# Kernel tuning notes

Measured on AMD Instinct MI355X. Metric: run time of the kernel, lower is better.

The kernel has to match this reference:

```python
import jax, jax.numpy as jnp
import numpy as np

NUM_LEVELS = 4
RADIUS = 4


def _avg_pool2(x):
    # x: [N, H, W] -> 2x2 avg pool, stride 2, VALID (matches F.avg_pool2d(corr, 2, 2))
    s = jax.lax.reduce_window(x, 0.0, jax.lax.add, (1, 2, 2), (1, 2, 2), 'VALID')
    return s * 0.25


def _bilinear_sampler(img, coords):
    # img: [N, H, W]; coords: [N, K, K, 2] with (x, y) in pixel units.
    # Matches grid_sample(align_corners=True, padding_mode='zeros').
    N, H, W = img.shape
    x, y = coords[..., 0], coords[..., 1]
    x0 = jnp.floor(x)
    y0 = jnp.floor(y)
    nidx = jnp.arange(N)[:, None, None]

    def corner(xi, yi, w):
        valid = (xi >= 0) & (xi <= W - 1) & (yi >= 0) & (yi <= H - 1)
        xc = jnp.clip(xi, 0, W - 1).astype(jnp.int32)
        yc = jnp.clip(yi, 0, H - 1).astype(jnp.int32)
        return jnp.where(valid, img[nidx, yc, xc], 0.0) * w

    wx1 = x - x0
    wx0 = 1.0 - wx1
    wy1 = y - y0
    wy0 = 1.0 - wy1
    return (corner(x0, y0, wx0 * wy0) + corner(x0 + 1.0, y0, wx1 * wy0)
            + corner(x0, y0 + 1.0, wx0 * wy1) + corner(x0 + 1.0, y0 + 1.0, wx1 * wy1))


def setup_inputs() -> dict:
    key = jax.random.key(0)
    ks = jax.random.split(key, 8)
    B, C, H, W, D = 2, 256, 46, 96, 256
    fmap1 = jax.random.normal(ks[0], (B, C, H, W), jnp.float32)
    fmap2 = jax.random.normal(ks[1], (B, C, H, W), jnp.float32)
    ys, xs = jnp.meshgrid(jnp.arange(H, dtype=jnp.float32),
                          jnp.arange(W, dtype=jnp.float32), indexing='ij')
    base = jnp.broadcast_to(jnp.stack([xs, ys], 0), (B, 2, H, W))  # channels = (x, y)
    coords1 = base
    coords_lookup = base + 2.0 * jax.random.normal(ks[2], (B, 2, H, W), jnp.float32)
    Wf = jax.random.normal(ks[3], (C, D), jnp.float32) / np.sqrt(C).astype(np.float32)
    bf = jnp.zeros((D,), jnp.float32)
    Wpos = jax.random.normal(ks[4], (2, D), jnp.float32) * 0.003
    Wq = jax.random.normal(ks[5], (D, D), jnp.float32) / np.sqrt(D).astype(np.float32)
    Wk = jax.random.normal(ks[6], (D, D), jnp.float32) / np.sqrt(D).astype(np.float32)
    return {"fmap1": fmap1, "fmap2": fmap2, "coords1": coords1,
            "coords_lookup": coords_lookup, "Wf": Wf, "bf": bf,
            "Wpos": Wpos, "Wq": Wq, "Wk": Wk}


def reference(fmap1, fmap2, coords1, coords_lookup, Wf, bf, Wpos, Wq, Wk):
    B, C, H, W = fmap1.shape
    HW = H * W
    D = Wf.shape[1]
    dt = fmap1.dtype
    # --- update(): SETrans cross-attention correlation volume ---
    # coords2 = gen_all_indices -> full (y, x) grid
    ys, xs = jnp.meshgrid(jnp.arange(H, dtype=dt), jnp.arange(W, dtype=dt), indexing='ij')
    coords2_yx = jnp.broadcast_to(jnp.stack([ys, xs], -1), (B, H, W, 2)).reshape(B, HW, 2)
    # coords1 stored as (x, y) channels; permute(0,2,3,1).flip(-1) -> (y, x)
    coords1_yx = jnp.transpose(coords1, (0, 2, 3, 1))[..., ::-1].reshape(B, HW, 2)
    f1 = jnp.transpose(fmap1.reshape(B, C, HW), (0, 2, 1))  # [B, HW, C]
    f2 = jnp.transpose(fmap2.reshape(B, C, HW), (0, 2, 1))
    pos1 = coords1_yx @ Wpos                                  # [B, HW, D]
    pos2 = coords2_yx @ Wpos
    vispos1 = f1 @ Wf + bf + pos1
    vispos2 = f2 @ Wf + bf + pos2
    scale = jnp.sqrt(jnp.asarray(D, dt))
    pos_biases = jnp.einsum('bid,bjd->bij', pos1, pos2) / scale  # injected positional biases
    q = vispos1 @ Wq
    k = vispos2 @ Wk
    scores = jnp.einsum('bid,bjd->bij', q, k) / scale + pos_biases
    corr = jax.nn.softmax(scores, axis=-1)                    # [B, HW1, HW2] attn-prob correlation
    corr = corr.reshape(B * HW, H, W)
    pyramid = [corr]
    for _ in range(NUM_LEVELS - 1):
        corr = _avg_pool2(corr)
        pyramid.append(corr)
    # --- __call__(coords): multiscale bilinear lookup ---
    r = RADIUS
    d = jnp.linspace(-r, r, 2 * r + 1, dtype=dt)
    dyy, dxx = jnp.meshgrid(d, d, indexing='ij')              # matches torch.meshgrid(dy, dx)
    delta = jnp.stack([dyy, dxx], -1)[None]                   # [1, K, K, 2]
    cl = jnp.transpose(coords_lookup, (0, 2, 3, 1)).reshape(B * HW, 1, 1, 2)
    outs = []
    for i, lvl in enumerate(pyramid):
        coords_lvl = cl / (2.0 ** i) + delta                  # [B*HW, K, K, 2]
        samp = _bilinear_sampler(lvl, coords_lvl)             # [B*HW, K, K]
        outs.append(samp.reshape(B, H, W, -1))
    out = jnp.concatenate(outs, axis=-1)                      # [B, H, W, L*K*K]
    return jnp.transpose(out, (0, 3, 1, 2)).astype(jnp.float32)
```

## Files before the change

kernel.cpp:

```cpp
#include <hip/hip_runtime.h>
#include <cstdint>

typedef _Float16 f16;
typedef __attribute__((ext_vector_type(2))) _Float16 f16x2;
typedef __attribute__((ext_vector_type(4))) _Float16 f16x4;
typedef __attribute__((ext_vector_type(8))) _Float16 f16x8;
typedef __attribute__((ext_vector_type(4))) float f32x4;

#define NB 2
#define NH 46
#define NW 96
#define NHW 4416
#define ND 256
#define NTILES 276
#define SSTR 4424
#define L2E 1.44269504f

#define OFF_WFQ 0
#define OFF_WFK 131072
#define OFF_PQ  262144
#define OFF_PK  264192
#define OFF_BQ  266240
#define OFF_BK  267264
#define OFF_GS  268288
#define OFF_Q   268544
#define OFF_K   4790528
#define OFF_RM  9312512
#define OFF_S   9453824
#define SCOL    4432
#define WS_NEED 87740672UL

__global__ __launch_bounds__(256) void prep_kernel(
    const float* __restrict__ Wf, const float* __restrict__ bf,
    const float* __restrict__ Wpos, const float* __restrict__ Wq,
    const float* __restrict__ Wk, char* __restrict__ ws) {
  f16* WFQ = (f16*)(ws + OFF_WFQ);
  f16* WFK = (f16*)(ws + OFF_WFK);
  float* PQ = (float*)(ws + OFF_PQ);
  float* PK = (float*)(ws + OFF_PK);
  float* BQ = (float*)(ws + OFF_BQ);
  float* BK = (float*)(ws + OFF_BK);
  float* GS = (float*)(ws + OFF_GS);
  int bid = blockIdx.x, d = threadIdx.x;
  if (bid < 256) {
    int c = bid;
    float aq = 0.f, ak = 0.f;
    for (int t = 0; t < 256; ++t) {
      float wf = Wf[c * 256 + t];
      aq += wf * Wq[t * 256 + d];
      ak += wf * Wk[t * 256 + d];
    }
    WFQ[c * 256 + d] = (f16)(aq * 0.0625f);
    WFK[c * 256 + d] = (f16)ak;
  } else if (bid == 256) {
    float pq0 = 0, pq1 = 0, pk0 = 0, pk1 = 0, bq = 0, bk = 0;
    for (int c = 0; c < 256; ++c) {
      float wq = Wq[c * 256 + d], wk = Wk[c * 256 + d];
      pq0 += Wpos[c] * wq;       pq1 += Wpos[256 + c] * wq;
      pk0 += Wpos[c] * wk;       pk1 += Wpos[256 + c] * wk;
      bq  += bf[c] * wq;         bk  += bf[c] * wk;
    }
    PQ[d] = pq0 * 0.0625f; PQ[256 + d] = pq1 * 0.0625f;
    PK[d] = pk0;           PK[256 + d] = pk1;
    BQ[d] = bq * 0.0625f;  BK[d] = bk;
  } else if (d < 4) {
    int a = d >> 1, b2 = d & 1;
    float g = 0;
    for (int t = 0; t < 256; ++t) g += Wpos[a * 256 + t] * Wpos[b2 * 256 + t];
    GS[d] = g * 0.0625f;
  }
}

__global__ __launch_bounds__(256) void qk_gemm(
    const float* __restrict__ fmap1, const float* __restrict__ fmap2,
    const float* __restrict__ coords1, char* __restrict__ ws) {
  __shared__ f16 As[64 * 40];
  __shared__ f16 Bs[128 * 40];
  __shared__ float py[64], px[64];
  const int z = blockIdx.z;
  const float* fmap = z ? fmap2 : fmap1;
  const f16* Wt = (const f16*)(ws + (z ? OFF_WFK : OFF_WFQ));
  const float* P = (const float*)(ws + (z ? OFF_PK : OFF_PQ));
  const float* bias = (const float*)(ws + (z ? OFF_BK : OFF_BQ));
  f16* outb = (f16*)(ws + (z ? OFF_K : OFF_Q));
  const int t = threadIdx.x;
  const int g0 = blockIdx.x * 64;
  const int b = g0 / NHW;
  const int hwb = g0 - b * NHW;
  const int d0 = blockIdx.y * 128;
  if (t < 64) {
    int hw = hwb + t;
    if (z == 0) {
      py[t] = coords1[(b * 2 + 1) * NHW + hw];
      px[t] = coords1[(b * 2 + 0) * NHW + hw];
    } else {
      int y = hw / NW;
      py[t] = (float)y;
      px[t] = (float)(hw - y * NW);
    }
  }
  const int lane = t & 63, wave = t >> 6;
  const int wr = (wave >> 1) * 32, wc0 = (wave & 1) * 64;
  const int hwl = t & 63, cl0 = t >> 6;
  const int dd = t & 127, ch = t >> 7;
  f32x4 acc[2][4] = {};
  for (int kt = 0; kt < 8; ++kt) {
    int kk = kt * 32;
    __syncthreads();
#pragma unroll
    for (int i = 0; i < 8; ++i) {
      int c = cl0 + i * 4;
      As[hwl * 40 + c] = (f16)fmap[(size_t)(b * ND + kk + c) * NHW + hwb + hwl];
    }
#pragma unroll
    for (int i = 0; i < 16; ++i) {
      int c = ch * 16 + i;
      Bs[dd * 40 + c] = Wt[(kk + c) * ND + d0 + dd];
    }
    __syncthreads();
    int row = lane & 15, kq = (lane >> 4) * 8;
    f16x8 a0 = *(const f16x8*)&As[(wr + row) * 40 + kq];
    f16x8 a1 = *(const f16x8*)&As[(wr + 16 + row) * 40 + kq];
#pragma unroll
    for (int s = 0; s < 4; ++s) {
      f16x8 bs = *(const f16x8*)&Bs[(wc0 + 16 * s + row) * 40 + kq];
      acc[0][s] = __builtin_amdgcn_mfma_f32_16x16x32_f16(a0, bs, acc[0][s], 0, 0, 0);
      acc[1][s] = __builtin_amdgcn_mfma_f32_16x16x32_f16(a1, bs, acc[1][s], 0, 0, 0);
    }
  }
#pragma unroll
  for (int fi = 0; fi < 2; ++fi)
#pragma unroll
    for (int s = 0; s < 4; ++s)
#pragma unroll
      for (int r = 0; r < 4; ++r) {
        int rowl = wr + fi * 16 + (lane >> 4) * 4 + r;
        int d = d0 + wc0 + s * 16 + (lane & 15);
        float v = acc[fi][s][r] + bias[d] + py[rowl] * P[d] + px[rowl] * P[ND + d];
        outb[(size_t)(g0 + rowl) * ND + d] = (f16)v;
      }
}

__global__ __launch_bounds__(384, 2) void score_gemm(
    const float* __restrict__ coords1, char* __restrict__ ws) {
  __shared__ f16 kls[2][32][264];
  __shared__ f16 stw[6][16][36];
  __shared__ float u0s[96], u1s[96];
  const int tid = threadIdx.x;
  const int blk = blockIdx.x;
  const int xcd = blk & 7;
  const int b = xcd >> 2, nq = xcd & 3;
  const int hw0 = (blk >> 3) * 96;
  const int j00 = nq * 1104;
  const float* GS = (const float*)(ws + OFF_GS);
  if (tid < 96) {
    int hw = hw0 + tid;
    float cy = coords1[(b * 2 + 1) * NHW + hw];
    float cx = coords1[(b * 2 + 0) * NHW + hw];
    u0s[tid] = cy * GS[0] + cx * GS[2];
    u1s[tid] = cy * GS[1] + cx * GS[3];
  }
  const f16* __restrict__ qb = (const f16*)(ws + OFF_Q);
  const f16* __restrict__ kb = (const f16*)(ws + OFF_K);
  f16* __restrict__ gSb = (f16*)(ws + OFF_S) + ((size_t)b * NHW + hw0) * SCOL;
  float* __restrict__ rmG = (float*)(ws + OFF_RM);
  const int lane = tid & 63, wave = tid >> 6;
  const int q = lane & 15, h = lane >> 4;
  f16x8 qfrag[8];
#pragma unroll
  for (int ks = 0; ks < 8; ++ks)
    qfrag[ks] = *(const f16x8*)&qb[(size_t)(b * NHW + hw0 + wave * 16 + q) * ND + ks * 32 + h * 8];
  for (int c = tid; c < 32 * 32; c += 384) {
    int r = c >> 5, cc = c & 31;
    *(f16x8*)&kls[0][r][cc * 8] =
        *(const f16x8*)&kb[(size_t)(b * NHW + j00 + r) * ND + cc * 8];
  }
  __syncthreads();
  const float u0m = u0s[wave * 16 + q], u1m = u1s[wave * 16 + q];
  float pmax = -3e38f;
  const int srow = lane >> 2, scg = lane & 3;

  for (int it = 0; it <= 34; ++it) {
    const int buf = it & 1;
    const int jp = j00 + it * 32;
    const bool full = (it < 34);
    if (it < 34) {
      const int nW = (it < 33) ? 32 : 16;
      const int jn = j00 + (it + 1) * 32;
      for (int c = tid; c < nW * 32; c += 384) {
        int r = c >> 5, cc = c & 31;
        *(f16x8*)&kls[buf ^ 1][r][cc * 8] =
            *(const f16x8*)&kb[(size_t)(b * NHW + jn + r) * ND + cc * 8];
      }
    }
    f32x4 acc0 = {}, acc1 = {};
#pragma unroll
    for (int ks = 0; ks < 8; ++ks) {
      f16x8 kf = *(const f16x8*)&kls[buf][q][ks * 32 + h * 8];
      acc0 = __builtin_amdgcn_mfma_f32_16x16x32_f16(kf, qfrag[ks], acc0, 0, 0, 0);
    }
    if (full) {
#pragma unroll
      for (int ks = 0; ks < 8; ++ks) {
        f16x8 kf = *(const f16x8*)&kls[buf][16 + q][ks * 32 + h * 8];
        acc1 = __builtin_amdgcn_mfma_f32_16x16x32_f16(kf, qfrag[ks], acc1, 0, 0, 0);
      }
    }
    {
      f16x4 v0, v1;
#pragma unroll
      for (int r = 0; r < 4; ++r) {
        int j = jp + h * 4 + r;
        int yj = j / NW;
        float s = acc0[r] + u0m * (float)yj + u1m * (float)(j - yj * NW);
        pmax = fmaxf(pmax, s);
        v0[r] = (f16)s;
      }
      *(f16x4*)&stw[wave][q][h * 4] = v0;
      if (full) {
#pragma unroll
        for (int r = 0; r < 4; ++r) {
          int j = jp + 16 + h * 4 + r;
          int yj = j / NW;
          float s = acc1[r] + u0m * (float)yj + u1m * (float)(j - yj * NW);
          pmax = fmaxf(pmax, s);
          v1[r] = (f16)s;
        }
        *(f16x4*)&stw[wave][q][16 + h * 4] = v1;
      }
    }
    if (full) {
      f16x8 row8 = *(const f16x8*)&stw[wave][srow][scg * 8];
      *(f16x8*)&gSb[(size_t)(wave * 16 + srow) * SCOL + jp + scg * 8] = row8;
    } else {
      f16x4 row4 = *(const f16x4*)&stw[wave][srow][scg * 4];
      *(f16x4*)&gSb[(size_t)(wave * 16 + srow) * SCOL + jp + scg * 4] = row4;
    }
    __syncthreads();
  }
  pmax = fmaxf(pmax, __shfl_xor(pmax, 16));
  pmax = fmaxf(pmax, __shfl_xor(pmax, 32));
  if (lane < 16)
    rmG[((size_t)b * 4 + nq) * NHW + hw0 + wave * 16 + q] = pmax;
}

__global__ __launch_bounds__(512) void lookup_kernel(
    const float* __restrict__ clup, const char* __restrict__ ws,
    float* __restrict__ out) {
  __shared__ f16 lv1[4][1104];
  __shared__ f16 lv2[4][264];
  __shared__ f16 lv3[4][60];
  __shared__ float wpart[8];
  __shared__ float clxs[16], clys[16], rinv[16], rm[16];
  const int tid = threadIdx.x;
  const int blk0 = blockIdx.x;
  const int xcd = blk0 & 7;
  const int b = xcd >> 2;
  const int hw0 = ((blk0 >> 3) * 4 + (xcd & 3)) * 16;
  const f16* gS = (const f16*)(ws + OFF_S);
  const float* rmG = (const float*)(ws + OFF_RM);
  if (tid < 16) {
    int hw = hw0 + tid;
    clxs[tid] = clup[(b * 2 + 0) * NHW + hw];
    clys[tid] = clup[(b * 2 + 1) * NHW + hw];
    const float* rp = rmG + (size_t)b * 4 * NHW + hw;
    rm[tid] = fmaxf(fmaxf(rp[0], rp[NHW]), fmaxf(rp[2 * NHW], rp[3 * NHW]));
  }
  __syncthreads();
  const int lane = tid & 63, wave = tid >> 6;
  const int rgrp = tid >> 7, ts = tid & 127;
  for (int p = 0; p < 4; ++p) {
    const int r = p * 4 + rgrp;
    const f16* sp = gS + (size_t)(b * NHW + hw0 + r) * SCOL;
    const float m = rm[r];
    float psum = 0.f;
    for (int cp = ts; cp < 552; cp += 128) {
      int c = cp * 2;
      int yy = c / 48, xx = c - yy * 48;
      f16x4 a = *(const f16x4*)&sp[(2 * yy) * NW + 2 * xx];
      f16x4 bb = *(const f16x4*)&sp[(2 * yy + 1) * NW + 2 * xx];
      float e0 = __builtin_amdgcn_exp2f(((float)a[0] - m) * L2E);
      float e1 = __builtin_amdgcn_exp2f(((float)a[1] - m) * L2E);
      float e2 = __builtin_amdgcn_exp2f(((float)bb[0] - m) * L2E);
      float e3 = __builtin_amdgcn_exp2f(((float)bb[1] - m) * L2E);
      float e4 = __builtin_amdgcn_exp2f(((float)a[2] - m) * L2E);
      float e5 = __builtin_amdgcn_exp2f(((float)a[3] - m) * L2E);
      float e6 = __builtin_amdgcn_exp2f(((float)bb[2] - m) * L2E);
      float e7 = __builtin_amdgcn_exp2f(((float)bb[3] - m) * L2E);
      float sA = (e0 + e1) + (e2 + e3);
      float sB = (e4 + e5) + (e6 + e7);
      f16x2 w2; w2[0] = (f16)sA; w2[1] = (f16)sB;
      *(f16x2*)&lv1[rgrp][c] = w2;
      psum += sA + sB;
    }
#pragma unroll
    for (int off = 1; off < 64; off <<= 1) psum += __shfl_xor(psum, off);
    if (lane == 0) wpart[wave] = psum;
    __syncthreads();
    if (tid < 4)
      rinv[p * 4 + tid] = 1.f / (wpart[2 * tid] + wpart[2 * tid + 1]);
    for (int c2 = ts; c2 < 264; c2 += 128) {
      int yy = c2 / 24, xx = c2 - yy * 24;
      f16x2 a = *(const f16x2*)&lv1[rgrp][(2 * yy) * 48 + 2 * xx];
      f16x2 bb = *(const f16x2*)&lv1[rgrp][(2 * yy + 1) * 48 + 2 * xx];
      lv2[rgrp][c2] = (f16)(((float)a[0] + (float)a[1]) + ((float)bb[0] + (float)bb[1]));
    }
    __syncthreads();
    if (ts < 60) {
      int yy = ts / 12, xx = ts - yy * 12;
      f16x2 a = *(const f16x2*)&lv2[rgrp][(2 * yy) * 24 + 2 * xx];
      f16x2 bb = *(const f16x2*)&lv2[rgrp][(2 * yy + 1) * 24 + 2 * xx];
      lv3[rgrp][ts] = (f16)(((float)a[0] + (float)a[1]) + ((float)bb[0] + (float)bb[1]));
    }
    __syncthreads();
    for (int idx = tid; idx < 1296; idx += 512) {
      int rl = idx / 324, c = idx - rl * 324;
      int rr = p * 4 + rl;
      int lvl = c / 81, rem = c - lvl * 81;
      int k0 = rem / 9, k1 = rem - k0 * 9;
      const float wdiv[4] = {1.f, 0.25f, 0.0625f, 0.015625f};
      const int Wi[4] = {96, 48, 24, 12}, Hi[4] = {46, 23, 11, 5};
      float m2 = rm[rr];
      const f16* spq = gS + (size_t)(b * NHW + hw0 + rr) * SCOL;
      float xq = clxs[rr] / (float)(1 << lvl) + (float)(k0 - 4);
      float yq = clys[rr] / (float)(1 << lvl) + (float)(k1 - 4);
      float x0f = floorf(xq), y0f = floorf(yq);
      int x0 = (int)x0f, y0 = (int)y0f;
      float wx1 = xq - x0f, wx0 = 1.f - wx1;
      float wy1 = yq - y0f, wy0 = 1.f - wy1;
      int Wl = Wi[lvl], Hl = Hi[lvl];
      float v = 0.f;
#pragma unroll
      for (int dy = 0; dy < 2; ++dy)
#pragma unroll
        for (int dx = 0; dx < 2; ++dx) {
          int xi = x0 + dx, yi = y0 + dy;
          if (xi >= 0 && xi < Wl && yi >= 0 && yi < Hl) {
            float pv;
            if (lvl == 0)
              pv = __builtin_amdgcn_exp2f(((float)spq[yi * NW + xi] - m2) * L2E);
            else if (lvl == 1) pv = (float)lv1[rl][yi * 48 + xi];
            else if (lvl == 2) pv = (float)lv2[rl][yi * 24 + xi];
            else               pv = (float)lv3[rl][yi * 12 + xi];
            v += pv * (dx ? wx1 : wx0) * (dy ? wy1 : wy0);
          }
        }
      int hw = hw0 + rr;
      int h = hw / NW, w = hw - h * NW;
      int chn = lvl * 81 + k0 * 9 + k1;
      out[((size_t)(b * 324 + chn) * NH + h) * NW + w] = v * wdiv[lvl] * rinv[rr];
    }
    __syncthreads();
  }
}

__global__ __launch_bounds__(1024) void attn_lookup(
    const float* __restrict__ coords1, const float* __restrict__ clup,
    const char* __restrict__ ws, float* __restrict__ out) {
  __shared__ f16 S[16 * SSTR];
  __shared__ f16 lv1[4][1104];
  __shared__ f16 lv2[4][264];
  __shared__ f16 lv3[4][60];
  __shared__ float wmax[16][16];
  __shared__ float wpart[16];
  __shared__ float u0s[16], u1s[16], clxs[16], clys[16], rinv[16], rowmaxS[16];
  const int tid = threadIdx.x;
  const int blk0 = blockIdx.x;
  const int xcd = blk0 & 7;
  const int b = xcd >> 2;
  const int hw0 = ((blk0 >> 3) * 4 + (xcd & 3)) * 16;
  const float* GS = (const float*)(ws + OFF_GS);
  if (tid < 16) {
    int hw = hw0 + tid;
    float cy = coords1[(b * 2 + 1) * NHW + hw];
    float cx = coords1[(b * 2 + 0) * NHW + hw];
    u0s[tid] = cy * GS[0] + cx * GS[2];
    u1s[tid] = cy * GS[1] + cx * GS[3];
    clxs[tid] = clup[(b * 2 + 0) * NHW + hw];
    clys[tid] = clup[(b * 2 + 1) * NHW + hw];
  }
  const f16* qb = (const f16*)(ws + OFF_Q);
  const f16* kb = (const f16*)(ws + OFF_K);
  const int lane = tid & 63;
  const int arow = lane & 15, akq = (lane >> 4) * 8;
  const int i0 = (lane >> 4) * 4;
  f16x8 afrag[8];
#pragma unroll
  for (int ks = 0; ks < 8; ++ks)
    afrag[ks] = *(const f16x8*)&qb[(size_t)(b * NHW + hw0 + arow) * ND + ks * 32 + akq];
  __syncthreads();
  float u0r[4], u1r[4];
#pragma unroll
  for (int r = 0; r < 4; ++r) { u0r[r] = u0s[i0 + r]; u1r[r] = u1s[i0 + r]; }
  const int wave = tid >> 6;
  float pmax[4] = {-3e38f, -3e38f, -3e38f, -3e38f};
  {
    const int cnt = (NTILES - wave + 15) / 16;
    const f16* kp = &kb[(size_t)(b * NHW + wave * 16 + arow) * ND + akq];
    const size_t tstep = (size_t)256 * ND;
    int nt = wave;
    f16x8 h0[4], h1[4];
#pragma unroll
    for (int s = 0; s < 4; ++s) h0[s] = *(const f16x8*)&kp[s * 32];
    for (int i = 0; i < cnt; ++i) {
      f32x4 acc0 = {}, acc1 = {};
// ... 87 lines not shown
      const float wdiv[4] = {1.f, 0.25f, 0.0625f, 0.015625f};
      const int Wi[4] = {96, 48, 24, 12}, Hi[4] = {46, 23, 11, 5};
      float m2 = rowmaxS[rr];
      float xq = clxs[rr] / (float)(1 << lvl) + (float)(k0 - 4);
      float yq = clys[rr] / (float)(1 << lvl) + (float)(k1 - 4);
      float x0f = floorf(xq), y0f = floorf(yq);
      int x0 = (int)x0f, y0 = (int)y0f;
      float wx1 = xq - x0f, wx0 = 1.f - wx1;
      float wy1 = yq - y0f, wy0 = 1.f - wy1;
      int Wl = Wi[lvl], Hl = Hi[lvl];
      float v = 0.f;
#pragma unroll
      for (int dy = 0; dy < 2; ++dy)
#pragma unroll
        for (int dx = 0; dx < 2; ++dx) {
          int xi = x0 + dx, yi = y0 + dy;
          if (xi >= 0 && xi < Wl && yi >= 0 && yi < Hl) {
            float pv;
            if (lvl == 0)
              pv = __builtin_amdgcn_exp2f(((float)S[rr * SSTR + yi * NW + xi] - m2) * L2E);
            else if (lvl == 1) pv = (float)lv1[rl][yi * 48 + xi];
            else if (lvl == 2) pv = (float)lv2[rl][yi * 24 + xi];
            else               pv = (float)lv3[rl][yi * 12 + xi];
            v += pv * (dx ? wx1 : wx0) * (dy ? wy1 : wy0);
          }
        }
      int hw = hw0 + rr;
      int h = hw / NW, w = hw - h * NW;
      int chn = lvl * 81 + k0 * 9 + k1;
      out[((size_t)(b * 324 + chn) * NH + h) * NW + w] = v * wdiv[lvl] * rinv[rr];
    }
    __syncthreads();
  }
}

extern "C" void kernel_launch(void* const* d_in, const int* in_sizes, int n_in,
                              void* d_out, int out_size, void* d_ws, size_t ws_size,
                              hipStream_t stream) {
  const float* fmap1 = (const float*)d_in[0];
  const float* fmap2 = (const float*)d_in[1];
  const float* coords1 = (const float*)d_in[2];
  const float* clup = (const float*)d_in[3];
  const float* Wf = (const float*)d_in[4];
  const float* bf = (const float*)d_in[5];
  const float* Wpos = (const float*)d_in[6];
  const float* Wq = (const float*)d_in[7];
  const float* Wk = (const float*)d_in[8];
  char* ws = (char*)d_ws;
  float* out = (float*)d_out;

  prep_kernel<<<dim3(258), dim3(256), 0, stream>>>(Wf, bf, Wpos, Wq, Wk, ws);
  qk_gemm<<<dim3(138, 2, 2), dim3(256), 0, stream>>>(fmap1, fmap2, coords1, ws);
  if (ws_size >= (size_t)WS_NEED) {
    score_gemm<<<dim3(46 * 8), dim3(384), 0, stream>>>(coords1, ws);
    lookup_kernel<<<dim3(NB * NTILES), dim3(512), 0, stream>>>(clup, ws, out);
  } else {
    attn_lookup<<<dim3(NB * NTILES), dim3(1024), 0, stream>>>(coords1, clup, ws, out);
  }
}
```

Before: 153.3 us.

## Give each score_gemm wave two query tiles and store K in fragment-native LDS layout

score_gemm now runs 3 waves instead of 6, and each wave owns 32 query rows, so every K fragment loaded from LDS feeds two MFMAs. K is staged in a pre-swizzled fragment-order layout, which lets each lane read one contiguous f16x8 without padded row indexing. The score tile writeback and row-max reduction are widened to match. Separately, the prep_kernel loops get unroll pragmas. Halving the threads per block lowers latency hiding and raises register pressure from the doubled q fragments and accumulators.

Result: slower. 188.0 us (+22.6%).

```diff
diff --git a/kernel.cpp b/kernel.cpp
--- a/kernel.cpp
+++ b/kernel.cpp
@@ -45,6 +45,7 @@
   if (bid < 256) {
     int c = bid;
     float aq = 0.f, ak = 0.f;
+#pragma unroll 8
     for (int t = 0; t < 256; ++t) {
       float wf = Wf[c * 256 + t];
       aq += wf * Wq[t * 256 + d];
@@ -54,6 +55,7 @@
     WFK[c * 256 + d] = (f16)ak;
   } else if (bid == 256) {
     float pq0 = 0, pq1 = 0, pk0 = 0, pk1 = 0, bq = 0, bk = 0;
+#pragma unroll 4
     for (int c = 0; c < 256; ++c) {
       float wq = Wq[c * 256 + d], wk = Wk[c * 256 + d];
       pq0 += Wpos[c] * wq;       pq1 += Wpos[256 + c] * wq;
@@ -141,10 +143,10 @@
       }
 }
 
-__global__ __launch_bounds__(384, 2) void score_gemm(
+__global__ __launch_bounds__(192, 2) void score_gemm(
     const float* __restrict__ coords1, char* __restrict__ ws) {
-  __shared__ f16 kls[2][32][264];
-  __shared__ f16 stw[6][16][36];
+  __shared__ f16x8 klsF[2][1024];
+  __shared__ f16 stw[3][32][40];
   __shared__ float u0s[96], u1s[96];
   const int tid = threadIdx.x;
   const int blk = blockIdx.x;
@@ -165,83 +167,94 @@
   f16* __restrict__ gSb = (f16*)(ws + OFF_S) + ((size_t)b * NHW + hw0) * SCOL;
   float* __restrict__ rmG = (float*)(ws + OFF_RM);
   const int lane = tid & 63, wave = tid >> 6;
-  const int q = lane & 15, h = lane >> 4;
-  f16x8 qfrag[8];
-#pragma unroll
-  for (int ks = 0; ks < 8; ++ks)
-    qfrag[ks] = *(const f16x8*)&qb[(size_t)(b * NHW + hw0 + wave * 16 + q) * ND + ks * 32 + h * 8];
-  for (int c = tid; c < 32 * 32; c += 384) {
-    int r = c >> 5, cc = c & 31;
-    *(f16x8*)&kls[0][r][cc * 8] =
-        *(const f16x8*)&kb[(size_t)(b * NHW + j00 + r) * ND + cc * 8];
+  const int lq = lane & 15, h = lane >> 4;
+  const int wq0 = wave * 32;
+  f16x8 qfrag[2][8];
+#pragma unroll
+  for (int s = 0; s < 2; ++s)
+#pragma unroll
+    for (int ks = 0; ks < 8; ++ks)
+      qfrag[s][ks] = *(const f16x8*)&qb[(size_t)(b * NHW + hw0 + wq0 + s * 16 + lq) * ND + ks * 32 + h * 8];
+  for (int c = tid; c < 1024; c += 192) {
+    int half = c >> 9, u = c & 511, ks = u >> 6, l = u & 63;
+    int r = half * 16 + (l & 15), col = ks * 32 + (l >> 4) * 8;
+    klsF[0][c] = *(const f16x8*)&kb[(size_t)(b * NHW + j00 + r) * ND + col];
   }
   __syncthreads();
-  const float u0m = u0s[wave * 16 + q], u1m = u1s[wave * 16 + q];
-  float pmax = -3e38f;
-  const int srow = lane >> 2, scg = lane & 3;
+  const float u0a = u0s[wq0 + lq], u1a = u1s[wq0 + lq];
+  const float u0b = u0s[wq0 + 16 + lq], u1b = u1s[wq0 + 16 + lq];
+  float pmax0 = -3e38f, pmax1 = -3e38f;
+  const int srow = lane >> 1, scg = lane & 1;
 
   for (int it = 0; it <= 34; ++it) {
     const int buf = it & 1;
     const int jp = j00 + it * 32;
     const bool full = (it < 34);
     if (it < 34) {
-      const int nW = (it < 33) ? 32 : 16;
+      const int nC = (it < 33) ? 1024 : 512;
       const int jn = j00 + (it + 1) * 32;
-      for (int c = tid; c < nW * 32; c += 384) {
-        int r = c >> 5, cc = c & 31;
-        *(f16x8*)&kls[buf ^ 1][r][cc * 8] =
-            *(const f16x8*)&kb[(size_t)(b * NHW + jn + r) * ND + cc * 8];
-      }
-    }
-    f32x4 acc0 = {}, acc1 = {};
+      for (int c = tid; c < nC; c += 192) {
+        int half = c >> 9, u = c & 511, ks = u >> 6, l = u & 63;
+        int r = half * 16 + (l & 15), col = ks * 32 + (l >> 4) * 8;
+        klsF[buf ^ 1][c] = *(const f16x8*)&kb[(size_t)(b * NHW + jn + r) * ND + col];
+      }
+    }
+    f32x4 acc[2][2] = {};
 #pragma unroll
     for (int ks = 0; ks < 8; ++ks) {
-      f16x8 kf = *(const f16x8*)&kls[buf][q][ks * 32 + h * 8];
-      acc0 = __builtin_amdgcn_mfma_f32_16x16x32_f16(kf, qfrag[ks], acc0, 0, 0, 0);
+      f16x8 k0 = klsF[buf][ks * 64 + lane];
+      acc[0][0] = __builtin_amdgcn_mfma_f32_16x16x32_f16(k0, qfrag[0][ks], acc[0][0], 0, 0, 0);
+      acc[0][1] = __builtin_amdgcn_mfma_f32_16x16x32_f16(k0, qfrag[1][ks], acc[0][1], 0, 0, 0);
     }
     if (full) {
 #pragma unroll
       for (int ks = 0; ks < 8; ++ks) {
-        f16x8 kf = *(const f16x8*)&kls[buf][16 + q][ks * 32 + h * 8];
-        acc1 = __builtin_amdgcn_mfma_f32_16x16x32_f16(kf, qfrag[ks], acc1, 0, 0, 0);
-      }
-    }
-    {
+        f16x8 k1 = klsF[buf][512 + ks * 64 + lane];
+        acc[1][0] = __builtin_amdgcn_mfma_f32_16x16x32_f16(k1, qfrag[0][ks], acc[1][0], 0, 0, 0);
+        acc[1][1] = __builtin_amdgcn_mfma_f32_16x16x32_f16(k1, qfrag[1][ks], acc[1][1], 0, 0, 0);
+      }
+    }
+    const int na = full ? 2 : 1;
+    for (int a = 0; a < na; ++a) {
+      float yf[4], xf[4];
+#pragma unroll
+      for (int r = 0; r < 4; ++r) {
+        int j = jp + a * 16 + h * 4 + r;
+        int yj = j / NW;
+        yf[r] = (float)yj; xf[r] = (float)(j - yj * NW);
+      }
       f16x4 v0, v1;
 #pragma unroll
       for (int r = 0; r < 4; ++r) {
-        int j = jp + h * 4 + r;
-        int yj = j / NW;
-        float s = acc0[r] + u0m * (float)yj + u1m * (float)(j - yj * NW);
-        pmax = fmaxf(pmax, s);
-        v0[r] = (f16)s;
-      }
-      *(f16x4*)&stw[wave][q][h * 4] = v0;
-      if (full) {
-#pragma unroll
-        for (int r = 0; r < 4; ++r) {
-          int j = jp + 16 + h * 4 + r;
-          int yj = j / NW;
-          float s = acc1[r] + u0m * (float)yj + u1m * (float)(j - yj * NW);
-          pmax = fmaxf(pmax, s);
-          v1[r] = (f16)s;
-        }
-        *(f16x4*)&stw[wave][q][16 + h * 4] = v1;
-      }
+        float s0 = acc[a][0][r] + u0a * yf[r] + u1a * xf[r];
+        float s1 = acc[a][1][r] + u0b * yf[r] + u1b * xf[r];
+        pmax0 = fmaxf(pmax0, s0);
+        pmax1 = fmaxf(pmax1, s1);
+        v0[r] = (f16)s0; v1[r] = (f16)s1;
+      }
+      *(f16x4*)&stw[wave][lq][a * 16 + h * 4] = v0;
+      *(f16x4*)&stw[wave][16 + lq][a * 16 + h * 4] = v1;
     }
     if (full) {
+#pragma unroll
+      for (int g = 0; g < 2; ++g) {
+        f16x8 row8 = *(const f16x8*)&stw[wave][srow][(scg * 2 + g) * 8];
+        *(f16x8*)&gSb[(size_t)(wq0 + srow) * SCOL + jp + (scg * 2 + g) * 8] = row8;
+      }
+    } else {
       f16x8 row8 = *(const f16x8*)&stw[wave][srow][scg * 8];
-      *(f16x8*)&gSb[(size_t)(wave * 16 + srow) * SCOL + jp + scg * 8] = row8;
-    } else {
-      f16x4 row4 = *(const f16x4*)&stw[wave][srow][scg * 4];
-      *(f16x4*)&gSb[(size_t)(wave * 16 + srow) * SCOL + jp + scg * 4] = row4;
-    }
-    __syncthreads();
-  }
-  pmax = fmaxf(pmax, __shfl_xor(pmax, 16));
-  pmax = fmaxf(pmax, __shfl_xor(pmax, 32));
-  if (lane < 16)
-    rmG[((size_t)b * 4 + nq) * NHW + hw0 + wave * 16 + q] = pmax;
+      *(f16x8*)&gSb[(size_t)(wq0 + srow) * SCOL + jp + scg * 8] = row8;
+    }
+    __syncthreads();
+  }
+  pmax0 = fmaxf(pmax0, __shfl_xor(pmax0, 16));
+  pmax0 = fmaxf(pmax0, __shfl_xor(pmax0, 32));
+  pmax1 = fmaxf(pmax1, __shfl_xor(pmax1, 16));
+  pmax1 = fmaxf(pmax1, __shfl_xor(pmax1, 32));
+  if (lane < 16) {
+    rmG[((size_t)b * 4 + nq) * NHW + hw0 + wq0 + lq] = pmax0;
+    rmG[((size_t)b * 4 + nq) * NHW + hw0 + wq0 + 16 + lq] = pmax1;
+  }
 }
 
 __global__ __launch_bounds__(512) void lookup_kernel(
@@ -544,7 +557,7 @@
   prep_kernel<<<dim3(258), dim3(256), 0, stream>>>(Wf, bf, Wpos, Wq, Wk, ws);
   qk_gemm<<<dim3(138, 2, 2), dim3(256), 0, stream>>>(fmap1, fmap2, coords1, ws);
   if (ws_size >= (size_t)WS_NEED) {
-    score_gemm<<<dim3(46 * 8), dim3(384), 0, stream>>>(coords1, ws);
+    score_gemm<<<dim3(46 * 8), dim3(192), 0, stream>>>(coords1, ws);
     lookup_kernel<<<dim3(NB * NTILES), dim3(512), 0, stream>>>(clup, ws, out);
   } else {
     attn_lookup<<<dim3(NB * NTILES), dim3(1024), 0, stream>>>(coords1, clup, ws, out);
```

## Fuse level-1 pooling and lookup window extraction into score GEMM epilogue

Applied to the files above, without the earlier changes.

The score GEMM no longer writes the full fp16 score matrix to global memory. It processes two image rows at a time, computes per-row-pair maxima, writes exp-pooled level-1 values, and copies a 16x16 window of raw scores around each lookup point. The lookup kernel then rescales level 1 with the per-pair maxima and samples level 0 from that window, which removes a large global write and read in exchange for more epilogue work and extra synchronisation in the GEMM. The prep loops also get unroll pragmas.

Result: slower. 203.2 us (+32.5%).

```diff
diff --git a/kernel.cpp b/kernel.cpp
--- a/kernel.cpp
+++ b/kernel.cpp
@@ -25,10 +25,10 @@
 #define OFF_GS  268288
 #define OFF_Q   268544
 #define OFF_K   4790528
-#define OFF_RM  9312512
-#define OFF_S   9453824
-#define SCOL    4432
-#define WS_NEED 87740672UL
+#define OFF_MP  9312512
+#define OFF_WIN 10160384
+#define OFF_L1  14682368
+#define WS_NEED 35031296UL
 
 __global__ __launch_bounds__(256) void prep_kernel(
     const float* __restrict__ Wf, const float* __restrict__ bf,
@@ -45,6 +45,7 @@
   if (bid < 256) {
     int c = bid;
     float aq = 0.f, ak = 0.f;
+#pragma unroll 8
     for (int t = 0; t < 256; ++t) {
       float wf = Wf[c * 256 + t];
       aq += wf * Wq[t * 256 + d];
@@ -54,6 +55,7 @@
     WFK[c * 256 + d] = (f16)ak;
   } else if (bid == 256) {
     float pq0 = 0, pq1 = 0, pk0 = 0, pk1 = 0, bq = 0, bk = 0;
+#pragma unroll 4
     for (int c = 0; c < 256; ++c) {
       float wq = Wq[c * 256 + d], wk = Wk[c * 256 + d];
       pq0 += Wpos[c] * wq;       pq1 += Wpos[256 + c] * wq;
@@ -142,16 +144,22 @@
 }
 
 __global__ __launch_bounds__(384, 2) void score_gemm(
-    const float* __restrict__ coords1, char* __restrict__ ws) {
+    const float* __restrict__ coords1, const float* __restrict__ clup,
+    char* __restrict__ ws) {
   __shared__ f16 kls[2][32][264];
-  __shared__ f16 stw[6][16][36];
+  __shared__ f16 Sbuf[96][200];
   __shared__ float u0s[96], u1s[96];
+  __shared__ float mrowL[96];
+  __shared__ float clwx[96], clwy[96];
   const int tid = threadIdx.x;
   const int blk = blockIdx.x;
   const int xcd = blk & 7;
   const int b = xcd >> 2, nq = xcd & 3;
   const int hw0 = (blk >> 3) * 96;
-  const int j00 = nq * 1104;
+  const int y0q = nq * 12;
+  const int j00 = y0q * NW;
+  const int npairs = (nq == 3) ? 5 : 6;
+  const int G = npairs * 6;
   const float* GS = (const float*)(ws + OFF_GS);
   if (tid < 96) {
     int hw = hw0 + tid;
@@ -159,35 +167,36 @@
     float cx = coords1[(b * 2 + 0) * NHW + hw];
     u0s[tid] = cy * GS[0] + cx * GS[2];
     u1s[tid] = cy * GS[1] + cx * GS[3];
+    clwx[tid] = clup[(b * 2 + 0) * NHW + hw];
+    clwy[tid] = clup[(b * 2 + 1) * NHW + hw];
   }
   const f16* __restrict__ qb = (const f16*)(ws + OFF_Q);
   const f16* __restrict__ kb = (const f16*)(ws + OFF_K);
-  f16* __restrict__ gSb = (f16*)(ws + OFF_S) + ((size_t)b * NHW + hw0) * SCOL;
-  float* __restrict__ rmG = (float*)(ws + OFF_RM);
+  float* __restrict__ mpG = (float*)(ws + OFF_MP);
+  f16* __restrict__ winG = (f16*)(ws + OFF_WIN);
+  f16* __restrict__ l1G = (f16*)(ws + OFF_L1);
   const int lane = tid & 63, wave = tid >> 6;
-  const int q = lane & 15, h = lane >> 4;
+  const int lq = lane & 15, h = lane >> 4;
+  const int wq0 = wave * 16;
   f16x8 qfrag[8];
 #pragma unroll
   for (int ks = 0; ks < 8; ++ks)
-    qfrag[ks] = *(const f16x8*)&qb[(size_t)(b * NHW + hw0 + wave * 16 + q) * ND + ks * 32 + h * 8];
-  for (int c = tid; c < 32 * 32; c += 384) {
+    qfrag[ks] = *(const f16x8*)&qb[(size_t)(b * NHW + hw0 + wq0 + lq) * ND + ks * 32 + h * 8];
+  for (int c = tid; c < 1024; c += 384) {
     int r = c >> 5, cc = c & 31;
     *(f16x8*)&kls[0][r][cc * 8] =
         *(const f16x8*)&kb[(size_t)(b * NHW + j00 + r) * ND + cc * 8];
   }
   __syncthreads();
-  const float u0m = u0s[wave * 16 + q], u1m = u1s[wave * 16 + q];
+  const float u0m = u0s[wq0 + lq], u1m = u1s[wq0 + lq];
   float pmax = -3e38f;
-  const int srow = lane >> 2, scg = lane & 3;
-
-  for (int it = 0; it <= 34; ++it) {
-    const int buf = it & 1;
-    const int jp = j00 + it * 32;
-    const bool full = (it < 34);
-    if (it < 34) {
-      const int nW = (it < 33) ? 32 : 16;
-      const int jn = j00 + (it + 1) * 32;
-      for (int c = tid; c < nW * 32; c += 384) {
+
+  for (int g = 0; g < G; ++g) {
+    const int buf = g & 1;
+    const int jp = j00 + g * 32;
+    if (g + 1 < G) {
+      const int jn = j00 + (g + 1) * 32;
+      for (int c = tid; c < 1024; c += 384) {
         int r = c >> 5, cc = c & 31;
         *(f16x8*)&kls[buf ^ 1][r][cc * 8] =
             *(const f16x8*)&kb[(size_t)(b * NHW + jn + r) * ND + cc * 8];
@@ -196,52 +205,75 @@
     f32x4 acc0 = {}, acc1 = {};
 #pragma unroll
     for (int ks = 0; ks < 8; ++ks) {
-      f16x8 kf = *(const f16x8*)&kls[buf][q][ks * 32 + h * 8];
-      acc0 = __builtin_amdgcn_mfma_f32_16x16x32_f16(kf, qfrag[ks], acc0, 0, 0, 0);
-    }
-    if (full) {
-#pragma unroll
-      for (int ks = 0; ks < 8; ++ks) {
-        f16x8 kf = *(const f16x8*)&kls[buf][16 + q][ks * 32 + h * 8];
-        acc1 = __builtin_amdgcn_mfma_f32_16x16x32_f16(kf, qfrag[ks], acc1, 0, 0, 0);
-      }
-    }
-    {
-      f16x4 v0, v1;
+      f16x8 kA = *(const f16x8*)&kls[buf][lq][ks * 32 + h * 8];
+      acc0 = __builtin_amdgcn_mfma_f32_16x16x32_f16(kA, qfrag[ks], acc0, 0, 0, 0);
+    }
+#pragma unroll
+    for (int ks = 0; ks < 8; ++ks) {
+      f16x8 kA = *(const f16x8*)&kls[buf][16 + lq][ks * 32 + h * 8];
+      acc1 = __builtin_amdgcn_mfma_f32_16x16x32_f16(kA, qfrag[ks], acc1, 0, 0, 0);
+    }
+    const int c0 = (g % 6) * 32;
+#pragma unroll
+    for (int a = 0; a < 2; ++a) {
+      f16x4 v;
+      f32x4 ac = a ? acc1 : acc0;
 #pragma unroll
       for (int r = 0; r < 4; ++r) {
-        int j = jp + h * 4 + r;
+        int j = jp + a * 16 + h * 4 + r;
         int yj = j / NW;
-        float s = acc0[r] + u0m * (float)yj + u1m * (float)(j - yj * NW);
+        float s = ac[r] + u0m * (float)yj + u1m * (float)(j - yj * NW);
         pmax = fmaxf(pmax, s);
-        v0[r] = (f16)s;
-      }
-      *(f16x4*)&stw[wave][q][h * 4] = v0;
-      if (full) {
-#pragma unroll
-        for (int r = 0; r < 4; ++r) {
-          int j = jp + 16 + h * 4 + r;
-          int yj = j / NW;
-          float s = acc1[r] + u0m * (float)yj + u1m * (float)(j - yj * NW);
-          pmax = fmaxf(pmax, s);
-          v1[r] = (f16)s;
+        v[r] = (f16)s;
+      }
+      *(f16x4*)&Sbuf[wq0 + lq][c0 + a * 16 + h * 4] = v;
+    }
+    __syncthreads();
+    if ((g % 6) == 5) {
+      const int t = g / 6;
+      const int y1g = nq * 6 + t;
+      float pm = fmaxf(pmax, __shfl_xor(pmax, 16));
+      pm = fmaxf(pm, __shfl_xor(pm, 32));
+      if (lane < 16) mrowL[wq0 + lq] = pm;
+      __syncthreads();
+      {
+        const int row = tid >> 2, xq = tid & 3;
+        const float m = mrowL[row];
+        size_t rowbase = (size_t)(b * NHW + hw0 + row) * 1152 + (size_t)y1g * 48;
+#pragma unroll
+        for (int x4 = 0; x4 < 3; ++x4) {
+          f16x4 v;
+#pragma unroll
+          for (int e = 0; e < 4; ++e) {
+            int x = xq * 12 + x4 * 4 + e;
+            float e00 = __builtin_amdgcn_exp2f(((float)Sbuf[row][2 * x] - m) * L2E);
+            float e01 = __builtin_amdgcn_exp2f(((float)Sbuf[row][2 * x + 1] - m) * L2E);
+            float e10 = __builtin_amdgcn_exp2f(((float)Sbuf[row][96 + 2 * x] - m) * L2E);
+            float e11 = __builtin_amdgcn_exp2f(((float)Sbuf[row][96 + 2 * x + 1] - m) * L2E);
+            v[e] = (f16)((e00 + e01) + (e10 + e11));
+          }
+          *(f16x4*)&l1G[rowbase + xq * 12 + x4 * 4] = v;
         }
-        *(f16x4*)&stw[wave][q][16 + h * 4] = v1;
-      }
-    }
-    if (full) {
-      f16x8 row8 = *(const f16x8*)&stw[wave][srow][scg * 8];
-      *(f16x8*)&gSb[(size_t)(wave * 16 + srow) * SCOL + jp + scg * 8] = row8;
-    } else {
-      f16x4 row4 = *(const f16x4*)&stw[wave][srow][scg * 4];
-      *(f16x4*)&gSb[(size_t)(wave * 16 + srow) * SCOL + jp + scg * 4] = row4;
-    }
-    __syncthreads();
-  }
-  pmax = fmaxf(pmax, __shfl_xor(pmax, 16));
-  pmax = fmaxf(pmax, __shfl_xor(pmax, 32));
-  if (lane < 16)
-    rmG[((size_t)b * 4 + nq) * NHW + hw0 + wave * 16 + q] = pmax;
+        if (xq == 0) mpG[(size_t)(b * NHW + hw0 + row) * 24 + y1g] = m;
+      }
+      if (tid < 192) {
+        const int row = tid >> 1, sy = tid & 1;
+        const int yy = y0q + 2 * t + sy;
+        int wy0 = (int)floorf(clwy[row]) - 4;
+        wy0 = wy0 < 0 ? 0 : (wy0 > 30 ? 30 : wy0);
+        if (yy >= wy0 && yy < wy0 + 16) {
+          int wx0 = (int)floorf(clwx[row]) - 4;
+          wx0 = wx0 < 0 ? 0 : (wx0 > 80 ? 80 : wx0);
+          size_t wb = ((size_t)(b * NHW + hw0 + row) * 16 + (yy - wy0)) * 16;
+#pragma unroll
+          for (int e = 0; e < 16; ++e)
+            winG[wb + e] = Sbuf[row][sy * 96 + wx0 + e];
+        }
+      }
+      pmax = -3e38f;
+      __syncthreads();
+    }
+  }
 }
 
 __global__ __launch_bounds__(512) void lookup_kernel(
@@ -250,48 +282,51 @@
   __shared__ f16 lv1[4][1104];
   __shared__ f16 lv2[4][264];
   __shared__ f16 lv3[4][60];
+  __shared__ f16 winL[4][256];
+  __shared__ float mpl[4][23];
+  __shared__ float rowmL[4][4];
   __shared__ float wpart[8];
-  __shared__ float clxs[16], clys[16], rinv[16], rm[16];
+  __shared__ float clxs[16], clys[16], rinv[16];
   const int tid = threadIdx.x;
   const int blk0 = blockIdx.x;
   const int xcd = blk0 & 7;
   const int b = xcd >> 2;
   const int hw0 = ((blk0 >> 3) * 4 + (xcd & 3)) * 16;
-  const f16* gS = (const f16*)(ws + OFF_S);
-  const float* rmG = (const float*)(ws + OFF_RM);
+  const float* mpG = (const float*)(ws + OFF_MP);
+  const f16* winG = (const f16*)(ws + OFF_WIN);
+  const f16* l1G = (const f16*)(ws + OFF_L1);
   if (tid < 16) {
     int hw = hw0 + tid;
     clxs[tid] = clup[(b * 2 + 0) * NHW + hw];
     clys[tid] = clup[(b * 2 + 1) * NHW + hw];
-    const float* rp = rmG + (size_t)b * 4 * NHW + hw;
-    rm[tid] = fmaxf(fmaxf(rp[0], rp[NHW]), fmaxf(rp[2 * NHW], rp[3 * NHW]));
   }
   __syncthreads();
   const int lane = tid & 63, wave = tid >> 6;
   const int rgrp = tid >> 7, ts = tid & 127;
   for (int p = 0; p < 4; ++p) {
     const int r = p * 4 + rgrp;
-    const f16* sp = gS + (size_t)(b * NHW + hw0 + r) * SCOL;
-    const float m = rm[r];
+    const size_t grow = (size_t)(b * NHW + hw0 + r);
+    if (ts < 23) mpl[rgrp][ts] = mpG[grow * 24 + ts];
+    if (ts >= 32 && ts < 64) {
+      int w8 = ts - 32;
+      *(f16x8*)&winL[rgrp][w8 * 8] = *(const f16x8*)&winG[grow * 256 + w8 * 8];
+    }
+    __syncthreads();
+    float m = mpl[rgrp][0];
+#pragma unroll
+    for (int t = 1; t < 23; ++t) m = fmaxf(m, mpl[rgrp][t]);
+    if (ts == 0) rowmL[rgrp][0] = m;
+    const f16* l1r = &l1G[grow * 1152];
     float psum = 0.f;
     for (int cp = ts; cp < 552; cp += 128) {
       int c = cp * 2;
-      int yy = c / 48, xx = c - yy * 48;
-      f16x4 a = *(const f16x4*)&sp[(2 * yy) * NW + 2 * xx];
-      f16x4 bb = *(const f16x4*)&sp[(2 * yy + 1) * NW + 2 * xx];
-      float e0 = __builtin_amdgcn_exp2f(((float)a[0] - m) * L2E);
-      float e1 = __builtin_amdgcn_exp2f(((float)a[1] - m) * L2E);
-      float e2 = __builtin_amdgcn_exp2f(((float)bb[0] - m) * L2E);
-      float e3 = __builtin_amdgcn_exp2f(((float)bb[1] - m) * L2E);
-      float e4 = __builtin_amdgcn_exp2f(((float)a[2] - m) * L2E);
-      float e5 = __builtin_amdgcn_exp2f(((float)a[3] - m) * L2E);
-      float e6 = __builtin_amdgcn_exp2f(((float)bb[2] - m) * L2E);
-      float e7 = __builtin_amdgcn_exp2f(((float)bb[3] - m) * L2E);
-      float sA = (e0 + e1) + (e2 + e3);
-      float sB = (e4 + e5) + (e6 + e7);
-      f16x2 w2; w2[0] = (f16)sA; w2[1] = (f16)sB;
+      int y1 = cp / 24;
+      float ef = __builtin_amdgcn_exp2f((mpl[rgrp][y1] - m) * L2E);
+      f16x2 v = *(const f16x2*)&l1r[c];
+      float a0 = (float)v[0] * ef, a1 = (float)v[1] * ef;
+      f16x2 w2; w2[0] = (f16)a0; w2[1] = (f16)a1;
       *(f16x2*)&lv1[rgrp][c] = w2;
-      psum += sA + sB;
+      psum += a0 + a1;
     }
 #pragma unroll
     for (int off = 1; off < 64; off <<= 1) psum += __shfl_xor(psum, off);
@@ -320,8 +355,6 @@
       int k0 = rem / 9, k1 = rem - k0 * 9;
       const float wdiv[4] = {1.f, 0.25f, 0.0625f, 0.015625f};
       const int Wi[4] = {96, 48, 24, 12}, Hi[4] = {46, 23, 11, 5};
-      float m2 = rm[rr];
-      const f16* spq = gS + (size_t)(b * NHW + hw0 + rr) * SCOL;
       float xq = clxs[rr] / (float)(1 << lvl) + (float)(k0 - 4);
       float yq = clys[rr] / (float)(1 << lvl) + (float)(k1 - 4);
       float x0f = floorf(xq), y0f = floorf(yq);
@@ -330,6 +363,11 @@
       float wy1 = yq - y0f, wy0 = 1.f - wy1;
       int Wl = Wi[lvl], Hl = Hi[lvl];
       float v = 0.f;
+      float m2 = rowmL[rl][0];
+      int wy0i = (int)floorf(clys[rr]) - 4;
+      wy0i = wy0i < 0 ? 0 : (wy0i > 30 ? 30 : wy0i);
+      int wx0i = (int)floorf(clxs[rr]) - 4;
+      wx0i = wx0i < 0 ? 0 : (wx0i > 80 ? 80 : wx0i);
 #pragma unroll
       for (int dy = 0; dy < 2; ++dy)
 #pragma unroll
@@ -338,7 +376,8 @@
           if (xi >= 0 && xi < Wl && yi >= 0 && yi < Hl) {
             float pv;
             if (lvl == 0)
-              pv = __builtin_amdgcn_exp2f(((float)spq[yi * NW + xi] - m2) * L2E);
+              pv = __builtin_amdgcn_exp2f(
+                  ((float)winL[rl][(yi - wy0i) * 16 + (xi - wx0i)] - m2) * L2E);
             else if (lvl == 1) pv = (float)lv1[rl][yi * 48 + xi];
             else if (lvl == 2) pv = (float)lv2[rl][yi * 24 + xi];
             else               pv = (float)lv3[rl][yi * 12 + xi];
@@ -346,9 +385,9 @@
           }
         }
       int hw = hw0 + rr;
-      int h = hw / NW, w = hw - h * NW;
+      int hh = hw / NW, wcol = hw - hh * NW;
       int chn = lvl * 81 + k0 * 9 + k1;
-      out[((size_t)(b * 324 + chn) * NH + h) * NW + w] = v * wdiv[lvl] * rinv[rr];
+      out[((size_t)(b * 324 + chn) * NH + hh) * NW + wcol] = v * wdiv[lvl] * rinv[rr];
     }
     __syncthreads();
   }
@@ -544,7 +583,7 @@
   prep_kernel<<<dim3(258), dim3(256), 0, stream>>>(Wf, bf, Wpos, Wq, Wk, ws);
   qk_gemm<<<dim3(138, 2, 2), dim3(256), 0, stream>>>(fmap1, fmap2, coords1, ws);
   if (ws_size >= (size_t)WS_NEED) {
-    score_gemm<<<dim3(46 * 8), dim3(384), 0, stream>>>(coords1, ws);
+    score_gemm<<<dim3(46 * 8), dim3(384), 0, stream>>>(coords1, clup, ws);
     lookup_kernel<<<dim3(NB * NTILES), dim3(512), 0, stream>>>(clup, ws, out);
   } else {
     attn_lookup<<<dim3(NB * NTILES), dim3(1024), 0, stream>>>(coords1, clup, ws, out);
```

## Restructure lookup kernel to one wave per row with wave-local pyramids

Applied to the files above, without the earlier changes.

Each wave in the lookup kernel now owns two query rows end to end. It builds that row's pooled pyramid levels in its own LDS slice and reduces the softmax denominator with wave shuffles, so block-wide __syncthreads are replaced by wave-local fences. Level-0 bilinear taps now read from a small LDS window, staged once per row around the lookup point, instead of scattered global loads. Pool loads are widened to 8-element vectors, and unroll pragmas are added to the prep-kernel loops. The design relies on wave-lockstep visibility of LDS writes and uses more LDS per block, which may reduce occupancy.

Result: faster. 149.5 us (-2.5%).

```diff
diff --git a/kernel.cpp b/kernel.cpp
--- a/kernel.cpp
+++ b/kernel.cpp
@@ -45,6 +45,7 @@
   if (bid < 256) {
     int c = bid;
     float aq = 0.f, ak = 0.f;
+#pragma unroll 8
     for (int t = 0; t < 256; ++t) {
       float wf = Wf[c * 256 + t];
       aq += wf * Wq[t * 256 + d];
@@ -54,6 +55,7 @@
     WFK[c * 256 + d] = (f16)ak;
   } else if (bid == 256) {
     float pq0 = 0, pq1 = 0, pk0 = 0, pk1 = 0, bq = 0, bk = 0;
+#pragma unroll 4
     for (int c = 0; c < 256; ++c) {
       float wq = Wq[c * 256 + d], wk = Wk[c * 256 + d];
       pq0 += Wpos[c] * wq;       pq1 += Wpos[256 + c] * wq;
@@ -247,11 +249,10 @@
 __global__ __launch_bounds__(512) void lookup_kernel(
     const float* __restrict__ clup, const char* __restrict__ ws,
     float* __restrict__ out) {
-  __shared__ f16 lv1[4][1104];
-  __shared__ f16 lv2[4][264];
-  __shared__ f16 lv3[4][60];
-  __shared__ float wpart[8];
-  __shared__ float clxs[16], clys[16], rinv[16], rm[16];
+  __shared__ f16 lv1W[8][1104];
+  __shared__ f16 lv2W[8][264];
+  __shared__ f16 lv3W[8][60];
+  __shared__ f16 winW[8][10][24];
   const int tid = threadIdx.x;
   const int blk0 = blockIdx.x;
   const int xcd = blk0 & 7;
@@ -259,75 +260,87 @@
   const int hw0 = ((blk0 >> 3) * 4 + (xcd & 3)) * 16;
   const f16* gS = (const f16*)(ws + OFF_S);
   const float* rmG = (const float*)(ws + OFF_RM);
-  if (tid < 16) {
-    int hw = hw0 + tid;
-    clxs[tid] = clup[(b * 2 + 0) * NHW + hw];
-    clys[tid] = clup[(b * 2 + 1) * NHW + hw];
+  const int lane = tid & 63, wave = tid >> 6;
+  f16* lv1 = lv1W[wave];
+  f16* lv2 = lv2W[wave];
+  f16* lv3 = lv3W[wave];
+
+  for (int rr2 = 0; rr2 < 2; ++rr2) {
+    const int r = wave * 2 + rr2;
+    const int hw = hw0 + r;
+    const size_t grow = (size_t)b * NHW + hw;
+    const f16* sp = gS + grow * SCOL;
+    const float clx = clup[(b * 2 + 0) * NHW + hw];
+    const float cly = clup[(b * 2 + 1) * NHW + hw];
     const float* rp = rmG + (size_t)b * 4 * NHW + hw;
-    rm[tid] = fmaxf(fmaxf(rp[0], rp[NHW]), fmaxf(rp[2 * NHW], rp[3 * NHW]));
-  }
-  __syncthreads();
-  const int lane = tid & 63, wave = tid >> 6;
-  const int rgrp = tid >> 7, ts = tid & 127;
-  for (int p = 0; p < 4; ++p) {
-    const int r = p * 4 + rgrp;
-    const f16* sp = gS + (size_t)(b * NHW + hw0 + r) * SCOL;
-    const float m = rm[r];
+    const float m = fmaxf(fmaxf(rp[0], rp[NHW]), fmaxf(rp[2 * NHW], rp[3 * NHW]));
+    const int wy0 = (int)floorf(cly) - 4;
+    const int wx0 = (int)floorf(clx) - 4;
+    const int xb = (wx0 >> 3) << 3;
+    if (lane < 30) {
+      int r10 = lane / 3, chk = lane - r10 * 3;
+      int yy = wy0 + r10;
+      int xc = xb + chk * 8;
+      if (yy >= 0 && yy < NH) {
+        if (xc >= 0 && xc + 8 <= NW) {
+          *(f16x8*)&winW[wave][r10][chk * 8] = *(const f16x8*)&sp[yy * NW + xc];
+        } else {
+#pragma unroll
+          for (int e = 0; e < 8; ++e) {
+            int x = xc + e;
+            winW[wave][r10][chk * 8 + e] =
+                (x >= 0 && x < NW) ? sp[yy * NW + x] : (f16)0.f;
+          }
+        }
+      }
+    }
     float psum = 0.f;
-    for (int cp = ts; cp < 552; cp += 128) {
-      int c = cp * 2;
-      int yy = c / 48, xx = c - yy * 48;
-      f16x4 a = *(const f16x4*)&sp[(2 * yy) * NW + 2 * xx];
-      f16x4 bb = *(const f16x4*)&sp[(2 * yy + 1) * NW + 2 * xx];
-      float e0 = __builtin_amdgcn_exp2f(((float)a[0] - m) * L2E);
-      float e1 = __builtin_amdgcn_exp2f(((float)a[1] - m) * L2E);
-      float e2 = __builtin_amdgcn_exp2f(((float)bb[0] - m) * L2E);
-      float e3 = __builtin_amdgcn_exp2f(((float)bb[1] - m) * L2E);
-      float e4 = __builtin_amdgcn_exp2f(((float)a[2] - m) * L2E);
-      float e5 = __builtin_amdgcn_exp2f(((float)a[3] - m) * L2E);
-      float e6 = __builtin_amdgcn_exp2f(((float)bb[2] - m) * L2E);
-      float e7 = __builtin_amdgcn_exp2f(((float)bb[3] - m) * L2E);
-      float sA = (e0 + e1) + (e2 + e3);
-      float sB = (e4 + e5) + (e6 + e7);
-      f16x2 w2; w2[0] = (f16)sA; w2[1] = (f16)sB;
-      *(f16x2*)&lv1[rgrp][c] = w2;
-      psum += sA + sB;
+    for (int u = lane; u < 276; u += 64) {
+      int y1 = u / 12, g = u - y1 * 12;
+      f16x8 A = *(const f16x8*)&sp[(2 * y1) * NW + g * 8];
+      f16x8 B = *(const f16x8*)&sp[(2 * y1 + 1) * NW + g * 8];
+      f16x4 v;
+#pragma unroll
+      for (int e = 0; e < 4; ++e) {
+        float e00 = __builtin_amdgcn_exp2f(((float)A[2 * e] - m) * L2E);
+        float e01 = __builtin_amdgcn_exp2f(((float)A[2 * e + 1] - m) * L2E);
+        float e10 = __builtin_amdgcn_exp2f(((float)B[2 * e] - m) * L2E);
+        float e11 = __builtin_amdgcn_exp2f(((float)B[2 * e + 1] - m) * L2E);
+        float s4 = (e00 + e01) + (e10 + e11);
+        v[e] = (f16)s4;
+        psum += s4;
+      }
+      *(f16x4*)&lv1[y1 * 48 + g * 4] = v;
     }
 #pragma unroll
     for (int off = 1; off < 64; off <<= 1) psum += __shfl_xor(psum, off);
-    if (lane == 0) wpart[wave] = psum;
-    __syncthreads();
-    if (tid < 4)
-      rinv[p * 4 + tid] = 1.f / (wpart[2 * tid] + wpart[2 * tid + 1]);
-    for (int c2 = ts; c2 < 264; c2 += 128) {
+    const float rinv = 1.f / psum;
+    __threadfence_block();
+    for (int c2 = lane; c2 < 264; c2 += 64) {
       int yy = c2 / 24, xx = c2 - yy * 24;
-      f16x2 a = *(const f16x2*)&lv1[rgrp][(2 * yy) * 48 + 2 * xx];
-      f16x2 bb = *(const f16x2*)&lv1[rgrp][(2 * yy + 1) * 48 + 2 * xx];
-      lv2[rgrp][c2] = (f16)(((float)a[0] + (float)a[1]) + ((float)bb[0] + (float)bb[1]));
-    }
-    __syncthreads();
-    if (ts < 60) {
-      int yy = ts / 12, xx = ts - yy * 12;
-      f16x2 a = *(const f16x2*)&lv2[rgrp][(2 * yy) * 24 + 2 * xx];
-      f16x2 bb = *(const f16x2*)&lv2[rgrp][(2 * yy + 1) * 24 + 2 * xx];
-      lv3[rgrp][ts] = (f16)(((float)a[0] + (float)a[1]) + ((float)bb[0] + (float)bb[1]));
-    }
-    __syncthreads();
-    for (int idx = tid; idx < 1296; idx += 512) {
-      int rl = idx / 324, c = idx - rl * 324;
-      int rr = p * 4 + rl;
+      f16x2 a = *(const f16x2*)&lv1[(2 * yy) * 48 + 2 * xx];
+      f16x2 bb = *(const f16x2*)&lv1[(2 * yy + 1) * 48 + 2 * xx];
+      lv2[c2] = (f16)(((float)a[0] + (float)a[1]) + ((float)bb[0] + (float)bb[1]));
+    }
+    __threadfence_block();
+    if (lane < 60) {
+      int yy = lane / 12, xx = lane - yy * 12;
+      f16x2 a = *(const f16x2*)&lv2[(2 * yy) * 24 + 2 * xx];
+      f16x2 bb = *(const f16x2*)&lv2[(2 * yy + 1) * 24 + 2 * xx];
+      lv3[lane] = (f16)(((float)a[0] + (float)a[1]) + ((float)bb[0] + (float)bb[1]));
+    }
+    __threadfence_block();
+    for (int c = lane; c < 324; c += 64) {
       int lvl = c / 81, rem = c - lvl * 81;
       int k0 = rem / 9, k1 = rem - k0 * 9;
       const float wdiv[4] = {1.f, 0.25f, 0.0625f, 0.015625f};
       const int Wi[4] = {96, 48, 24, 12}, Hi[4] = {46, 23, 11, 5};
-      float m2 = rm[rr];
-      const f16* spq = gS + (size_t)(b * NHW + hw0 + rr) * SCOL;
-      float xq = clxs[rr] / (float)(1 << lvl) + (float)(k0 - 4);
-      float yq = clys[rr] / (float)(1 << lvl) + (float)(k1 - 4);
+      float xq = clx / (float)(1 << lvl) + (float)(k0 - 4);
+      float yq = cly / (float)(1 << lvl) + (float)(k1 - 4);
       float x0f = floorf(xq), y0f = floorf(yq);
       int x0 = (int)x0f, y0 = (int)y0f;
-      float wx1 = xq - x0f, wx0 = 1.f - wx1;
-      float wy1 = yq - y0f, wy0 = 1.f - wy1;
+      float wx1 = xq - x0f, wx0f_ = 1.f - wx1;
+      float wy1 = yq - y0f, wy0f_ = 1.f - wy1;
       int Wl = Wi[lvl], Hl = Hi[lvl];
       float v = 0.f;
 #pragma unroll
@@ -338,19 +351,19 @@
           if (xi >= 0 && xi < Wl && yi >= 0 && yi < Hl) {
             float pv;
             if (lvl == 0)
-              pv = __builtin_amdgcn_exp2f(((float)spq[yi * NW + xi] - m2) * L2E);
-            else if (lvl == 1) pv = (float)lv1[rl][yi * 48 + xi];
-            else if (lvl == 2) pv = (float)lv2[rl][yi * 24 + xi];
-            else               pv = (float)lv3[rl][yi * 12 + xi];
-            v += pv * (dx ? wx1 : wx0) * (dy ? wy1 : wy0);
+              pv = __builtin_amdgcn_exp2f(
+                  ((float)winW[wave][yi - wy0][xi - xb] - m) * L2E);
+            else if (lvl == 1) pv = (float)lv1[yi * 48 + xi];
+            else if (lvl == 2) pv = (float)lv2[yi * 24 + xi];
+            else               pv = (float)lv3[yi * 12 + xi];
+            v += pv * (dx ? wx1 : wx0f_) * (dy ? wy1 : wy0f_);
           }
         }
-      int hw = hw0 + rr;
-      int h = hw / NW, w = hw - h * NW;
+      int hh = hw / NW, wcol = hw - hh * NW;
       int chn = lvl * 81 + k0 * 9 + k1;
-      out[((size_t)(b * 324 + chn) * NH + h) * NW + w] = v * wdiv[lvl] * rinv[rr];
-    }
-    __syncthreads();
+      out[((size_t)(b * 324 + chn) * NH + hh) * NW + wcol] = v * wdiv[lvl] * rinv;
+    }
+    __threadfence_block();
   }
 }
 
```
